# Performance work log

Hardware: AMD Instinct MI355X
Metric: run time of the kernel (lower is better)

Reference implementation:

```python
import jax, jax.numpy as jnp
import numpy as np

DIM = 1024
H = 16
D = DIM // H
CS = 64  # chunk_size
SCALE = D ** -0.5


def setup_inputs() -> dict:
    key = jax.random.key(0)
    k1, k2, k3 = jax.random.split(key, 3)
    B, N = 4, 4096
    x = jax.random.normal(k1, (B, N, DIM), dtype=jnp.float32)
    # torch nn.Linear(dim, 3*dim, bias=False): y = x @ W.T, W:[3*dim, dim].
    # We store the transposed layout W_qkv:[dim, 3*dim] so y = x @ W_qkv.
    W_qkv = jax.random.normal(k2, (DIM, 3 * DIM), dtype=jnp.float32) * (DIM ** -0.5)
    W_out = jax.random.normal(k3, (DIM, DIM), dtype=jnp.float32) * (DIM ** -0.5)
    return {"x": x, "W_qkv": W_qkv, "W_out": W_out}


def reference(x, W_qkv, W_out):
    B, N, C = x.shape
    qkv = (x @ W_qkv).reshape(B, N, 3, H, D)
    qkv = jnp.transpose(qkv, (2, 0, 3, 1, 4))  # [3,B,H,N,D]
    q, k, v = qkv[0], qkv[1], qkv[2]
    # N chosen divisible by CS, so no padding needed (pad=0 branch).
    nc = N // CS
    q = q.reshape(B, H, nc, CS, D)
    k = k.reshape(B, H, nc, CS, D)
    v = v.reshape(B, H, nc, CS, D)
    # Local quadratic attention within each chunk, causal mask.
    attn = jnp.einsum('bhcqd,bhckd->bhcqk', q, k) * SCALE
    mask = jnp.triu(jnp.ones((CS, CS), dtype=bool), k=1)
    attn = jnp.where(mask, jnp.float32(-65000.0), attn)
    attn = jax.nn.softmax(attn, axis=-1)
    out_local = jnp.einsum('bhcqk,bhckd->bhcqd', attn, v)
    # Cross-chunk linear term (num_chunks > 1): mean-pooled K/V, exclusive cumsum.
    chunk_k = k.mean(axis=3)  # [B,H,nc,D]
    chunk_v = v.mean(axis=3)
    cum_k = jnp.cumsum(chunk_k, axis=2)
    cum_v = jnp.cumsum(chunk_v, axis=2)
    zeros = jnp.zeros((B, H, 1, D), dtype=x.dtype)
    cum_k = jnp.concatenate([zeros, cum_k[:, :, :-1]], axis=2)
    cum_v = jnp.concatenate([zeros, cum_v[:, :, :-1]], axis=2)
    cross = jax.nn.sigmoid(jnp.einsum('bhcsd,bhcd->bhcs', q, cum_k) * SCALE)
    out = out_local + cross[..., None] * cum_v[:, :, :, None, :] * 0.5
    out = out.reshape(B, H, N, D)
    out = jnp.transpose(out, (0, 2, 1, 3)).reshape(B, N, C)
    return out @ W_out
```

## Files before the change

### kernel.cpp

```cpp
#include <hip/hip_runtime.h>
#include <stdint.h>

typedef __attribute__((ext_vector_type(4))) float f32x4;
typedef __attribute__((ext_vector_type(8))) short short8;
typedef unsigned short u16;

#define NH 16
#define HD 64
#define SEQ 4096
#define BATCH 4
#define NROWS (BATCH * SEQ)
#define DIMC 1024
#define QKVC 3072
#define SCALE 0.125f

__device__ __forceinline__ u16 f2bf(float f) {
  union { float f; uint32_t u; } v; v.f = f;
  uint32_t u = v.u;
  uint32_t r = (u + 0x7fffu + ((u >> 16) & 1u)) >> 16;
  return (u16)r;
}
__device__ __forceinline__ float bf2f(u16 h) {
  union { uint32_t u; float f; } v; v.u = ((uint32_t)h) << 16;
  return v.f;
}

__global__ __launch_bounds__(256) void cvt_kernel(const float* __restrict__ in,
                                                  u16* __restrict__ out, int n4) {
  int i = blockIdx.x * 256 + threadIdx.x;
  if (i >= n4) return;
  float4 v = ((const float4*)in)[i];
  ushort4 o;
  o.x = f2bf(v.x); o.y = f2bf(v.y); o.z = f2bf(v.z); o.w = f2bf(v.w);
  ((ushort4*)out)[i] = o;
}

__global__ __launch_bounds__(256) void transpose_cvt(const float* __restrict__ in,
                                                     u16* __restrict__ out, int R, int C) {
  __shared__ float t[32][33];
  int nbx = C >> 5;
  int bx = blockIdx.x % nbx, by = blockIdx.x / nbx;
  int r0 = by << 5, c0 = bx << 5;
  int tid = threadIdx.x;
#pragma unroll
  for (int i = 0; i < 4; i++) {
    int id = i * 256 + tid; int lr = id >> 5, lc = id & 31;
    t[lr][lc] = in[(size_t)(r0 + lr) * C + (c0 + lc)];
  }
  __syncthreads();
#pragma unroll
  for (int i = 0; i < 4; i++) {
    int id = i * 256 + tid; int lr = id >> 5, lc = id & 31;
    out[(size_t)(c0 + lr) * R + (r0 + lc)] = f2bf(t[lc][lr]);
  }
}

template <int OUT_BF16, int DO_SUMS>
__global__ __launch_bounds__(512, 2) void gemm_bt(const u16* __restrict__ A,
                                                  const u16* __restrict__ Bt,
                                                  void* __restrict__ Cv,
                                                  float* __restrict__ chk,
                                                  float* __restrict__ chv,
                                                  int M, int N, int K) {
  __shared__ __align__(16) u16 lds4[4][16384];
  int nbx = N >> 8;
  int nwg = gridDim.x;
  int bid = blockIdx.x;
  int cpx = nwg >> 3;
  int swz = (bid & 7) * cpx + (bid >> 3);
  int bx = swz % nbx, by = swz / nbx;
  int tid = threadIdx.x, lane = tid & 63, wv = tid >> 6;
  int wr = wv >> 2, wc = wv & 3;
  int lr = lane & 15, g = lane >> 4;
  int rxk = (g ^ ((lr >> 1) & 3)) << 3;
  int rsub4 = lane >> 2;
  int clog = (lane & 3) ^ ((lane >> 3) & 3);

  const u16* Ap = A + (size_t)(by * 256) * K;
  const u16* Bp = Bt + (size_t)(bx * 256) * K;

  f32x4 acc[8][4];
#pragma unroll
  for (int m = 0; m < 8; m++)
#pragma unroll
    for (int n = 0; n < 4; n++) acc[m][n] = (f32x4){0.f, 0.f, 0.f, 0.f};

  short8 aA[8], bA[4], aB[8], bB[4];

#define ISSUE_A(L, T) do {                                                      \
    int ru_ = (L) * 128 + wv * 16;                                              \
    const u16* g_ = Ap + (size_t)(ru_ + rsub4) * K + (T) * 32 + clog * 8;       \
    __builtin_amdgcn_global_load_lds(                                           \
        (const __attribute__((address_space(1))) uint32_t*)g_,                  \
        (__attribute__((address_space(3))) uint32_t*)&lds4[(T) & 3][ru_ * 32],  \
        16, 0, 0);                                                              \
  } while (0)

#define ISSUE_B(L, T) do {                                                      \
    int ru_ = (L) * 128 + wv * 16;                                              \
    const u16* g_ = Bp + (size_t)(ru_ + rsub4) * K + (T) * 32 + clog * 8;       \
    __builtin_amdgcn_global_load_lds(                                           \
        (const __attribute__((address_space(1))) uint32_t*)g_,                  \
        (__attribute__((address_space(3)))                                      \
             uint32_t*)&lds4[(T) & 3][8192 + ru_ * 32],                         \
        16, 0, 0);                                                              \
  } while (0)

#define STAGE(T) do { ISSUE_A(0, T); ISSUE_A(1, T); ISSUE_B(0, T); ISSUE_B(1, T); } while (0)

#define READS(SA, SB, T) do {                                                   \
    const u16* ab_ = &lds4[(T) & 3][(wr * 128 + lr) * 32 + rxk];                \
    const u16* bb_ = &lds4[(T) & 3][8192 + (wc * 64 + lr) * 32 + rxk];          \
    _Pragma("unroll")                                                           \
    for (int m = 0; m < 8; m++) SA[m] = *(const short8*)(ab_ + m * 512);        \
    _Pragma("unroll")                                                           \
    for (int n = 0; n < 4; n++) SB[n] = *(const short8*)(bb_ + n * 512);        \
  } while (0)

#define MFMAS(SA, SB) do {                                                      \
    _Pragma("unroll")                                                           \
    for (int m = 0; m < 8; m++)                                                 \
      _Pragma("unroll")                                                         \
      for (int n = 0; n < 4; n++)                                               \
        acc[m][n] = __builtin_amdgcn_mfma_f32_16x16x32_bf16(                    \
            SA[m], SB[n], acc[m][n], 0, 0, 0);                                  \
  } while (0)

  int NT = K >> 5;
  STAGE(0); STAGE(1);
  __builtin_amdgcn_sched_barrier(0);
  asm volatile("s_waitcnt vmcnt(4)" ::: "memory");
  __builtin_amdgcn_s_barrier();
  READS(aA, bA, 0);
  __builtin_amdgcn_sched_barrier(0);

  for (int t = 0; t + 2 < NT; t += 2) {
    STAGE(t + 2);
    __builtin_amdgcn_sched_barrier(0);
    asm volatile("s_waitcnt vmcnt(4)" ::: "memory");
    __builtin_amdgcn_s_barrier();
    READS(aB, bB, t + 1);
    __builtin_amdgcn_sched_barrier(0);
    __builtin_amdgcn_s_setprio(1);
    MFMAS(aA, bA);
    __builtin_amdgcn_s_setprio(0);
    __builtin_amdgcn_sched_barrier(0);
    if (t + 3 < NT) STAGE(t + 3);
    __builtin_amdgcn_sched_barrier(0);
    if (t + 3 < NT) asm volatile("s_waitcnt vmcnt(4)" ::: "memory");
    else            asm volatile("s_waitcnt vmcnt(0)" ::: "memory");
    __builtin_amdgcn_s_barrier();
    READS(aA, bA, t + 2);
    __builtin_amdgcn_sched_barrier(0);
    __builtin_amdgcn_s_setprio(1);
    MFMAS(aB, bB);
    __builtin_amdgcn_s_setprio(0);
    __builtin_amdgcn_sched_barrier(0);
  }
  asm volatile("s_waitcnt vmcnt(0)" ::: "memory");
  __builtin_amdgcn_s_barrier();
  READS(aB, bB, NT - 1);
  __builtin_amdgcn_sched_barrier(0);
  __builtin_amdgcn_s_setprio(1);
  MFMAS(aA, bA);
  __builtin_amdgcn_sched_barrier(0);
  MFMAS(aB, bB);
  __builtin_amdgcn_s_setprio(0);

#undef ISSUE_A
#undef ISSUE_B
#undef STAGE
#undef READS
#undef MFMAS

  int rb = by * 256 + wr * 128, cb = bx * 256 + wc * 64;

  if (DO_SUMS && cb >= 1024) {
#pragma unroll
    for (int mh = 0; mh < 2; mh++)
#pragma unroll
      for (int n = 0; n < 4; n++) {
        float sum = 0.f;
#pragma unroll
        for (int m = mh * 4; m < mh * 4 + 4; m++)
#pragma unroll
          for (int r = 0; r < 4; r++) sum += acc[m][n][r];
        sum += __shfl_xor(sum, 16);
        sum += __shfl_xor(sum, 32);
        if (g == 0) {
          int grb = rb + mh * 64;
          int b = grb >> 12, c = (grb >> 6) & 63;
          int cg = cb + n * 16 + lr;
          int col = cg & 1023;
          int h = col >> 6, d = col & 63;
          float* dst = (cg < 2048) ? chk : chv;
          dst[(((size_t)(b * 16 + h)) * 64 + c) * 64 + d] = sum * 0.015625f;
        }
      }
  }

#pragma unroll
  for (int m = 0; m < 8; m++)
#pragma unroll
    for (int n = 0; n < 4; n++)
#pragma unroll
      for (int r = 0; r < 4; r++) {
        int rg = rb + m * 16 + g * 4 + r;
        int cg = cb + n * 16 + lr;
        float v = acc[m][n][r];
        if (OUT_BF16)
          ((u16*)Cv)[(size_t)rg * N + cg] = f2bf(v);
        else
          ((float*)Cv)[(size_t)rg * N + cg] = v;
      }
}

__global__ __launch_bounds__(256) void cumsum_excl(const float* __restrict__ ck,
                                                   const float* __restrict__ cv,
                                                   float* __restrict__ cuk,
                                                   float* __restrict__ cuv) {
  __shared__ float qk[4][64], qv[4][64];
  int bh = blockIdx.x;
  int d = threadIdx.x & 63, q = threadIdx.x >> 6;
  size_t base = ((size_t)bh * 64) * 64 + d;
  float sk = 0.f, sv = 0.f;
  for (int c = q * 16; c < q * 16 + 16; c++) {
    sk += ck[base + (size_t)c * 64];
    sv += cv[base + (size_t)c * 64];
  }
  qk[q][d] = sk; qv[q][d] = sv;
  __syncthreads();
  float ak = 0.f, av = 0.f;
  for (int p = 0; p < q; p++) { ak += qk[p][d]; av += qv[p][d]; }
  for (int c = q * 16; c < q * 16 + 16; c++) {
    size_t i = base + (size_t)c * 64;
    cuk[i] = ak; cuv[i] = av;
    ak += ck[i]; av += cv[i];
  }
}

__global__ __launch_bounds__(256) void attn_kernel(const u16* __restrict__ qkv,
                                                   const float* __restrict__ cuk,
                                                   const float* __restrict__ cuv,
                                                   u16* __restrict__ out) {
  int blk = blockIdx.x;
  int c = blk & 63, h = (blk >> 6) & 15, b = blk >> 10;
  int row0 = b * SEQ + c * 64;
  __shared__ u16 qp_s[64][88];
  __shared__ u16 k_s[64][88];
  __shared__ u16 vt_s[64][88];
  __shared__ u16 ck_s[64];
  __shared__ float cv_s[64];
  int tid = threadIdx.x;
  {
    if (tid < 64) {
      ck_s[tid] = f2bf(cuk[(size_t)blk * 64 + tid]);
      cv_s[tid] = cuv[(size_t)blk * 64 + tid];
    }
    int r = tid >> 2, qt = tid & 3;
    const u16* rp = qkv + (size_t)(row0 + r) * QKVC + h * 64 + qt * 16;
    uint4 q0 = *(const uint4*)rp;          uint4 q1 = *(const uint4*)(rp + 8);
    uint4 k0 = *(const uint4*)(rp + 1024); uint4 k1 = *(const uint4*)(rp + 1032);
    uint4 v0 = *(const uint4*)(rp + 2048); uint4 v1 = *(const uint4*)(rp + 2056);
    *(uint4*)&qp_s[r][qt * 16] = q0;    *(uint4*)&qp_s[r][qt * 16 + 8] = q1;
    *(uint4*)&k_s[r][qt * 16] = k0;     *(uint4*)&k_s[r][qt * 16 + 8] = k1;
    const u16* vv0 = (const u16*)&v0;   const u16* vv1 = (const u16*)&v1;
    int vcol = (r & 7) | ((((r >> 3) ^ qt) & 7) << 3);
#pragma unroll
    for (int j = 0; j < 8; j++) vt_s[qt * 16 + j][vcol] = vv0[j];
#pragma unroll
    for (int j = 0; j < 8; j++) vt_s[qt * 16 + 8 + j][vcol] = vv1[j];
  }
  __syncthreads();

  int lane = tid & 63, w = tid >> 6;
  int lr = lane & 15, g = lane >> 4;
  f32x4 accS[4];
#pragma unroll
  for (int n = 0; n < 4; n++) accS[n] = (f32x4){0.f, 0.f, 0.f, 0.f};
  f32x4 accC = (f32x4){0.f, 0.f, 0.f, 0.f};
  short8 zf = (short8){0, 0, 0, 0, 0, 0, 0, 0};
#pragma unroll
  for (int kt = 0; kt < 2; kt++) {
    int lk = kt * 32 + g * 8;
    short8 af = *(const short8*)&qp_s[w * 16 + lr][lk];
    short8 cf = (lr == 0) ? *(const short8*)&ck_s[lk] : zf;
    accC = __builtin_amdgcn_mfma_f32_16x16x32_bf16(af, cf, accC, 0, 0, 0);
#pragma unroll
    for (int n = 0; n < 4; n++) {
      short8 bf = *(const short8*)&k_s[n * 16 + lr][lk];
      accS[n] = __builtin_amdgcn_mfma_f32_16x16x32_bf16(af, bf, accS[n], 0, 0, 0);
    }
  }
  float crossv[4];
#pragma unroll
  for (int r4 = 0; r4 < 4; r4++) {
    int row = w * 16 + g * 4 + r4;
    float x[4];
    float mx = -3.4e38f;
#pragma unroll
    for (int n = 0; n < 4; n++) {
      int col = n * 16 + lr;
      x[n] = ((col & 63) > (row & 63)) ? -65000.0f : accS[n][r4] * SCALE;
      mx = fmaxf(mx, x[n]);
    }
    mx = fmaxf(mx, __shfl_xor(mx, 1));
    mx = fmaxf(mx, __shfl_xor(mx, 2));
    mx = fmaxf(mx, __shfl_xor(mx, 4));
    mx = fmaxf(mx, __shfl_xor(mx, 8));
    float p[4], sum = 0.f;
#pragma unroll
    for (int n = 0; n < 4; n++) { p[n] = __expf(x[n] - mx); sum += p[n]; }
    sum += __shfl_xor(sum, 1);
    sum += __shfl_xor(sum, 2);
    sum += __shfl_xor(sum, 4);
    sum += __shfl_xor(sum, 8);
    float inv = 1.0f / sum;
#pragma unroll
    for (int n = 0; n < 4; n++) qp_s[row][n * 16 + lr] = f2bf(p[n] * inv);
    float sg = 1.0f / (1.0f + __expf(-accC[r4] * SCALE));
    crossv[r4] = __shfl(sg, (lane & 48));
  }
  __syncthreads();
  f32x4 accO[4];
#pragma unroll
  for (int n = 0; n < 4; n++) accO[n] = (f32x4){0.f, 0.f, 0.f, 0.f};
#pragma unroll
  for (int kt = 0; kt < 2; kt++) {
    int lk = kt * 32 + g * 8;
    short8 pf = *(const short8*)&qp_s[w * 16 + lr][lk];
#pragma unroll
    for (int n = 0; n < 4; n++) {
      short8 vf = *(const short8*)&vt_s[n * 16 + lr][kt * 32 + ((g ^ n) << 3)];
      accO[n] = __builtin_amdgcn_mfma_f32_16x16x32_bf16(pf, vf, accO[n], 0, 0, 0);
    }
  }
#pragma unroll
  for (int n = 0; n < 4; n++)
#pragma unroll
    for (int r4 = 0; r4 < 4; r4++) {
      int row = w * 16 + g * 4 + r4;
      int col = n * 16 + lr;
      float v = accO[n][r4] + crossv[r4] * cv_s[col] * 0.5f;
      out[(size_t)(row0 + row) * DIMC + h * 64 + col] = f2bf(v);
    }
}

extern "C" void kernel_launch(void* const* d_in, const int* in_sizes, int n_in,
                              void* d_out, int out_size, void* d_ws, size_t ws_size,
                              hipStream_t stream) {
  const float* x = (const float*)d_in[0];
  const float* Wqkv = (const float*)d_in[1];
  const float* Wout = (const float*)d_in[2];
  char* ws = (char*)d_ws;
  size_t off = 0;
  auto alloc = [&](size_t b) {
    void* p = ws + off;
    off += (b + 255) & ~(size_t)255;
    return p;
  };
  u16* xb = (u16*)alloc((size_t)NROWS * DIMC * 2);
  u16* wqt = (u16*)alloc((size_t)QKVC * DIMC * 2);
  u16* wot = (u16*)alloc((size_t)DIMC * DIMC * 2);
  u16* qkvb = (u16*)alloc((size_t)NROWS * QKVC * 2);
  float* chk = (float*)alloc((size_t)4096 * 64 * 4);
  float* chv = (float*)alloc((size_t)4096 * 64 * 4);
  float* cuk = (float*)alloc((size_t)4096 * 64 * 4);
  float* cuv = (float*)alloc((size_t)4096 * 64 * 4);
  u16* attnb = xb;

  cvt_kernel<<<16384, 256, 0, stream>>>(x, xb, NROWS * DIMC / 4);
  transpose_cvt<<<3072, 256, 0, stream>>>(Wqkv, wqt, DIMC, QKVC);
  transpose_cvt<<<1024, 256, 0, stream>>>(Wout, wot, DIMC, DIMC);
  gemm_bt<1, 1><<<768, 512, 0, stream>>>(xb, wqt, qkvb, chk, chv, NROWS, QKVC, DIMC);
  cumsum_excl<<<64, 256, 0, stream>>>(chk, chv, cuk, cuv);
  attn_kernel<<<4096, 256, 0, stream>>>(qkvb, cuk, cuv, attnb);
  gemm_bt<0, 0><<<256, 512, 0, stream>>>(attnb, wot, d_out, nullptr, nullptr,
                                         NROWS, DIMC, DIMC);
}
```

Before: 205.8 us.

## Restructure GEMM main loop with A-prefetch double buffer and merge weight-transpose launches

The GEMM k-loop now runs one tile per iteration, using two A register buffers and a single B buffer. It loads B for the current tile and prefetches A for the next tile before issuing the MFMAs, with the MFMA loop reordered n-outer. This is meant to cut register pressure and overlap LDS reads with compute. The two weight transpose launches are merged into one kernel, and the x conversion kernel becomes grid-stride with fewer blocks, to save launch overhead. The loop hardcodes 32 k-tiles (K=1024), so the kernel only works for that K.

```diff
diff --git a/kernel.cpp b/kernel.cpp
--- a/kernel.cpp
+++ b/kernel.cpp
@@ -27,19 +27,26 @@
 
 __global__ __launch_bounds__(256) void cvt_kernel(const float* __restrict__ in,
                                                   u16* __restrict__ out, int n4) {
-  int i = blockIdx.x * 256 + threadIdx.x;
-  if (i >= n4) return;
-  float4 v = ((const float4*)in)[i];
-  ushort4 o;
-  o.x = f2bf(v.x); o.y = f2bf(v.y); o.z = f2bf(v.z); o.w = f2bf(v.w);
-  ((ushort4*)out)[i] = o;
-}
-
-__global__ __launch_bounds__(256) void transpose_cvt(const float* __restrict__ in,
-                                                     u16* __restrict__ out, int R, int C) {
+  int stride = gridDim.x * 256;
+  for (int i = blockIdx.x * 256 + threadIdx.x; i < n4; i += stride) {
+    float4 v = ((const float4*)in)[i];
+    ushort4 o;
+    o.x = f2bf(v.x); o.y = f2bf(v.y); o.z = f2bf(v.z); o.w = f2bf(v.w);
+    ((ushort4*)out)[i] = o;
+  }
+}
+
+__global__ __launch_bounds__(256) void transpose_cvt2(const float* __restrict__ wqkv,
+                                                      u16* __restrict__ wqt,
+                                                      const float* __restrict__ wout,
+                                                      u16* __restrict__ wot) {
   __shared__ float t[32][33];
+  const float* in; u16* out; int C, blk;
+  if (blockIdx.x < 3072) { in = wqkv; out = wqt; C = 3072; blk = blockIdx.x; }
+  else                   { in = wout; out = wot; C = 1024; blk = blockIdx.x - 3072; }
+  int R = 1024;
   int nbx = C >> 5;
-  int bx = blockIdx.x % nbx, by = blockIdx.x / nbx;
+  int bx = blk % nbx, by = blk / nbx;
   int r0 = by << 5, c0 = bx << 5;
   int tid = threadIdx.x;
 #pragma unroll
@@ -85,7 +92,7 @@
 #pragma unroll
     for (int n = 0; n < 4; n++) acc[m][n] = (f32x4){0.f, 0.f, 0.f, 0.f};
 
-  short8 aA[8], bA[4], aB[8], bB[4];
+  short8 aP0[8], aP1[8], b[4];
 
 #define ISSUE_A(L, T) do {                                                      \
     int ru_ = (L) * 128 + wv * 16;                                              \
@@ -108,69 +115,55 @@
 
 #define STAGE(T) do { ISSUE_A(0, T); ISSUE_A(1, T); ISSUE_B(0, T); ISSUE_B(1, T); } while (0)
 
-#define READS(SA, SB, T) do {                                                   \
+#define LDApre(SA, T) do {                                                      \
     const u16* ab_ = &lds4[(T) & 3][(wr * 128 + lr) * 32 + rxk];                \
+    _Pragma("unroll")                                                           \
+    for (int m = 0; m < 8; m++) SA[m] = *(const short8*)(ab_ + m * 512);        \
+  } while (0)
+
+#define LDBt(T) do {                                                            \
     const u16* bb_ = &lds4[(T) & 3][8192 + (wc * 64 + lr) * 32 + rxk];          \
     _Pragma("unroll")                                                           \
-    for (int m = 0; m < 8; m++) SA[m] = *(const short8*)(ab_ + m * 512);        \
+    for (int n = 0; n < 4; n++) b[n] = *(const short8*)(bb_ + n * 512);         \
+  } while (0)
+
+#define MFMAS(SA) do {                                                          \
     _Pragma("unroll")                                                           \
-    for (int n = 0; n < 4; n++) SB[n] = *(const short8*)(bb_ + n * 512);        \
-  } while (0)
-
-#define MFMAS(SA, SB) do {                                                      \
-    _Pragma("unroll")                                                           \
-    for (int m = 0; m < 8; m++)                                                 \
+    for (int n = 0; n < 4; n++)                                                 \
       _Pragma("unroll")                                                         \
-      for (int n = 0; n < 4; n++)                                               \
+      for (int m = 0; m < 8; m++)                                               \
         acc[m][n] = __builtin_amdgcn_mfma_f32_16x16x32_bf16(                    \
-            SA[m], SB[n], acc[m][n], 0, 0, 0);                                  \
-  } while (0)
-
-  int NT = K >> 5;
+            SA[m], b[n], acc[m][n], 0, 0, 0);                                   \
+  } while (0)
+
   STAGE(0); STAGE(1);
   __builtin_amdgcn_sched_barrier(0);
   asm volatile("s_waitcnt vmcnt(4)" ::: "memory");
   __builtin_amdgcn_s_barrier();
-  READS(aA, bA, 0);
+  LDApre(aP0, 0);
   __builtin_amdgcn_sched_barrier(0);
 
-  for (int t = 0; t + 2 < NT; t += 2) {
-    STAGE(t + 2);
+#pragma unroll 4
+  for (int t = 0; t < 32; t++) {
+    if (t + 2 < 32) STAGE(t + 2);
     __builtin_amdgcn_sched_barrier(0);
-    asm volatile("s_waitcnt vmcnt(4)" ::: "memory");
+    if (t + 2 < 32) asm volatile("s_waitcnt vmcnt(4)" ::: "memory");
+    else            asm volatile("s_waitcnt vmcnt(0)" ::: "memory");
     __builtin_amdgcn_s_barrier();
-    READS(aB, bB, t + 1);
+    LDBt(t);
+    if (t + 1 < 32) { if ((t & 1) == 0) LDApre(aP1, t + 1); else LDApre(aP0, t + 1); }
     __builtin_amdgcn_sched_barrier(0);
     __builtin_amdgcn_s_setprio(1);
-    MFMAS(aA, bA);
+    if ((t & 1) == 0) MFMAS(aP0); else MFMAS(aP1);
     __builtin_amdgcn_s_setprio(0);
     __builtin_amdgcn_sched_barrier(0);
-    if (t + 3 < NT) STAGE(t + 3);
-    __builtin_amdgcn_sched_barrier(0);
-    if (t + 3 < NT) asm volatile("s_waitcnt vmcnt(4)" ::: "memory");
-    else            asm volatile("s_waitcnt vmcnt(0)" ::: "memory");
-    __builtin_amdgcn_s_barrier();
-    READS(aA, bA, t + 2);
-    __builtin_amdgcn_sched_barrier(0);
-    __builtin_amdgcn_s_setprio(1);
-    MFMAS(aB, bB);
-    __builtin_amdgcn_s_setprio(0);
-    __builtin_amdgcn_sched_barrier(0);
-  }
-  asm volatile("s_waitcnt vmcnt(0)" ::: "memory");
-  __builtin_amdgcn_s_barrier();
-  READS(aB, bB, NT - 1);
-  __builtin_amdgcn_sched_barrier(0);
-  __builtin_amdgcn_s_setprio(1);
-  MFMAS(aA, bA);
-  __builtin_amdgcn_sched_barrier(0);
-  MFMAS(aB, bB);
-  __builtin_amdgcn_s_setprio(0);
+  }
 
 #undef ISSUE_A
 #undef ISSUE_B
 #undef STAGE
-#undef READS
+#undef LDApre
+#undef LDBt
 #undef MFMAS
 
   int rb = by * 256 + wr * 128, cb = bx * 256 + wc * 64;
@@ -189,12 +182,12 @@
         sum += __shfl_xor(sum, 32);
         if (g == 0) {
           int grb = rb + mh * 64;
-          int b = grb >> 12, c = (grb >> 6) & 63;
+          int b_ = grb >> 12, c = (grb >> 6) & 63;
           int cg = cb + n * 16 + lr;
           int col = cg & 1023;
           int h = col >> 6, d = col & 63;
           float* dst = (cg < 2048) ? chk : chv;
-          dst[(((size_t)(b * 16 + h)) * 64 + c) * 64 + d] = sum * 0.015625f;
+          dst[(((size_t)(b_ * 16 + h)) * 64 + c) * 64 + d] = sum * 0.015625f;
         }
       }
   }
@@ -369,9 +362,8 @@
   float* cuv = (float*)alloc((size_t)4096 * 64 * 4);
   u16* attnb = xb;
 
-  cvt_kernel<<<16384, 256, 0, stream>>>(x, xb, NROWS * DIMC / 4);
-  transpose_cvt<<<3072, 256, 0, stream>>>(Wqkv, wqt, DIMC, QKVC);
-  transpose_cvt<<<1024, 256, 0, stream>>>(Wout, wot, DIMC, DIMC);
+  cvt_kernel<<<2048, 256, 0, stream>>>(x, xb, NROWS * DIMC / 4);
+  transpose_cvt2<<<4096, 256, 0, stream>>>(Wqkv, wqt, Wout, wot);
   gemm_bt<1, 1><<<768, 512, 0, stream>>>(xb, wqt, qkvb, chk, chv, NROWS, QKVC, DIMC);
   cumsum_excl<<<64, 256, 0, stream>>>(chk, chv, cuk, cuv);
   attn_kernel<<<4096, 256, 0, stream>>>(qkvb, cuk, cuv, attnb);
```

Measured after the change: 268.7 us. 1.31x slower.
